# Kernel optimization log

Measured on AMD Instinct MI355X. Metric: run time of the kernel, lower is better.

## Reference

```python
import jax, jax.numpy as jnp
import numpy as np

B, S = 32, 4096
HID, MEM, ATT = 512, 512, 512


def setup_inputs() -> dict:
    key = jax.random.key(0)
    k1, k2, k3, k4, k5, k6, k7 = jax.random.split(key, 7)
    scale_h = 1.0 / np.sqrt(HID)
    scale_m = 1.0 / np.sqrt(MEM)
    scale_a = 1.0 / np.sqrt(ATT)
    return {
        "hidden": jax.random.normal(k1, (B, HID), dtype=jnp.float32),
        "memory": jax.random.normal(k2, (B, S, MEM), dtype=jnp.float32),
        "mem_pad": jnp.zeros((B, S), dtype=jnp.bool_),
        "coverage": jax.random.uniform(k3, (B, S), dtype=jnp.float32),
        # params stored as (in, out) so x @ W == torch Linear(x)
        "W_h": jax.random.uniform(k4, (HID, ATT), minval=-scale_h, maxval=scale_h, dtype=jnp.float32),
        "W_m": jax.random.uniform(k5, (MEM, ATT), minval=-scale_m, maxval=scale_m, dtype=jnp.float32),
        "W_c": jax.random.uniform(k6, (ATT,), minval=-1.0, maxval=1.0, dtype=jnp.float32),
        "v": jax.random.uniform(k7, (ATT,), minval=-scale_a, maxval=scale_a, dtype=jnp.float32),
    }


def reference(hidden, memory, mem_pad, coverage, W_h, W_m, W_c, v):
    h = hidden @ W_h                                   # (B, A)
    m = jnp.einsum('bsd,da->bsa', memory, W_m)         # (B, S, A)
    c_feat = coverage[..., None] * W_c                 # (B, S, A) ; Linear(1->A) == scalar * weight row
    score = jnp.einsum('bsa,a->bs', jnp.tanh(h[:, None, :] + m + c_feat), v)  # (B, S)
    score = jnp.where(mem_pad, -jnp.inf, score)
    attn_weights = jax.nn.softmax(score, axis=-1)      # (B, S)
    context = jnp.einsum('bs,bsd->bd', attn_weights, memory)  # (B, D)
    return context, attn_weights
```

## Files before the change

### kernel.cpp

```cpp
#include <hip/hip_runtime.h>
#include <hip/hip_bf16.h>
#include <math.h>

#define BB 32
#define SS 4096
#define DMEM 512
#define DATT 512

typedef short short8 __attribute__((ext_vector_type(8)));
typedef float floatx4 __attribute__((ext_vector_type(4)));

__device__ inline short f2bf(float x) {
    unsigned u = __float_as_uint(x);
    unsigned r = (u + 0x7fffu + ((u >> 16) & 1u)) >> 16;
    return (short)(r & 0xffffu);
}

__device__ inline float fast_tanh(float x) {
    float e = __expf(2.0f * x);
    float r = __builtin_amdgcn_rcpf(e + 1.0f);
    return __builtin_fmaf(-2.0f, r, 1.0f);
}

__device__ inline void gld_lds16(const void* g, void* l) {
    __builtin_amdgcn_global_load_lds(
        (const __attribute__((address_space(1))) unsigned int*)g,
        (__attribute__((address_space(3))) unsigned int*)l, 16, 0, 0);
}


__global__ void prep_wt_kernel(const float* __restrict__ Wm, short* __restrict__ Wt) {
    const int n0 = blockIdx.x * 32;
    const int k0 = blockIdx.y * 32;
    const int t = threadIdx.x;
    const int r = t >> 5, c = t & 31;
    __shared__ float lds[32 * 33];
#pragma unroll
    for (int j = 0; j < 4; ++j) {
        int kk = r + j * 8;
        lds[kk * 33 + c] = Wm[(size_t)(k0 + kk) * 512 + n0 + c];
    }
    __syncthreads();
#pragma unroll
    for (int j = 0; j < 4; ++j) {
        int nn = r + j * 8;
        Wt[(size_t)(n0 + nn) * 512 + k0 + c] = f2bf(lds[c * 33 + nn]);
    }
}

__global__ void prep_h_kernel(const float* __restrict__ hidden, const float* __restrict__ Wh,
                              float* __restrict__ h) {
    const int b = blockIdx.x;
    const int n = blockIdx.y * 256 + threadIdx.x;
    const int kc = blockIdx.z;
    float acc = 0.f;
#pragma unroll 8
    for (int k = kc * 128; k < kc * 128 + 128; ++k)
        acc += hidden[b * 512 + k] * Wh[(size_t)k * 512 + n];
    atomicAdd(&h[b * 512 + n], acc);
}


__global__ __launch_bounds__(1024, 4)
void fused_kernel(const float* __restrict__ memory,
                  const float* __restrict__ coverage,
                  const unsigned char* __restrict__ pad,
                  const short* __restrict__ Wt,
                  const float* __restrict__ h,
                  const float* __restrict__ Wc,
                  const float* __restrict__ v,
                  float* __restrict__ pOut,
                  float* __restrict__ mWS,
                  float* __restrict__ lWS,
                  float* __restrict__ ctxPart) {
    const int blk = blockIdx.x;
    const int b = blk >> 5;
    const int st = blk & 31;
    const int s0 = st * 128;

    const int tid = threadIdx.x;
    const int lane = tid & 63;
    const int wave = tid >> 6;
    const int wm = wave & 1;
    const int wn = wave >> 1;
    const int col = lane & 15;
    const int q = lane >> 4;

    __shared__ __align__(16) char smem[79368];
    char* tileB0 = smem;
    char* tileB1 = smem + 32768;
    char* tileA  = smem + 65536;
    float* covS   = (float*)(smem + 73728);
    float* sred   = (float*)(smem + 74240);
    float* scoreS = (float*)(smem + 78336);
    float* pS     = (float*)(smem + 78848);
    float* mlS    = (float*)(smem + 79360);
    float4* red4  = (float4*)smem;

    if (tid < 128) covS[tid] = coverage[(size_t)b * SS + s0 + tid];

    const float4* gA4 = (const float4*)(memory + ((size_t)b * SS + s0) * 512);
    const char* gB = (const char*)Wt;

    const int arow = tid >> 3, al8 = tid & 7;
    const int aoff = arow * 64 + (((al8 >> 1) ^ ((arow >> 1) & 3)) << 4) + ((al8 & 1) << 3);
    float4 apf;

    floatx4 acc[4][4];
#pragma unroll
    for (int mi = 0; mi < 4; ++mi)
#pragma unroll
        for (int ni = 0; ni < 4; ++ni)
            acc[mi][ni] = (floatx4){0.f, 0.f, 0.f, 0.f};

    apf = gA4[(size_t)arow * 128 + al8];
#pragma unroll
    for (int it = 0; it < 2; ++it) {
        int ci = it * 1024 + tid;
        int row = ci >> 2;
        int gch = (ci & 3) ^ ((row >> 1) & 3);
        gld_lds16(gB + (size_t)row * 1024 + gch * 16,
                  tileB0 + it * 16384 + wave * 1024);
    }
    {
        union { __hip_bfloat162 h2; unsigned u; } p0, p1;
        p0.h2 = __float22bfloat162_rn(make_float2(apf.x, apf.y));
        p1.h2 = __float22bfloat162_rn(make_float2(apf.z, apf.w));
        uint2 w; w.x = p0.u; w.y = p1.u;
        *(uint2*)(tileA + aoff) = w;
    }
    __syncthreads();

    for (int kt = 0; kt < 16; ++kt) {
        if (kt < 15) {
            apf = gA4[(size_t)arow * 128 + (kt + 1) * 8 + al8];
            char* ldsB = ((kt + 1) & 1) ? tileB1 : tileB0;
#pragma unroll
            for (int it = 0; it < 2; ++it) {
                int ci = it * 1024 + tid;
                int row = ci >> 2;
                int gch = (ci & 3) ^ ((row >> 1) & 3);
                gld_lds16(gB + (size_t)row * 1024 + (kt + 1) * 64 + gch * 16,
                          ldsB + it * 16384 + wave * 1024);
            }
        }

        const char* bbase = (kt & 1) ? tileB1 : tileB0;
        short8 af[4], bf[4];
#pragma unroll
        for (int mi = 0; mi < 4; ++mi) {
            int row = wm * 64 + mi * 16 + col;
            af[mi] = *(const short8*)(tileA + row * 64 + ((q ^ ((row >> 1) & 3)) << 4));
        }
#pragma unroll
        for (int ni = 0; ni < 4; ++ni) {
            int row = wn * 64 + ni * 16 + col;
            bf[ni] = *(const short8*)(bbase + row * 64 + ((q ^ ((row >> 1) & 3)) << 4));
        }
#pragma unroll
        for (int mi = 0; mi < 4; ++mi)
#pragma unroll
            for (int ni = 0; ni < 4; ++ni)
                acc[mi][ni] = __builtin_amdgcn_mfma_f32_16x16x32_bf16(af[mi], bf[ni], acc[mi][ni], 0, 0, 0);

        __syncthreads();

        if (kt < 15) {
            union { __hip_bfloat162 h2; unsigned u; } p0, p1;
            p0.h2 = __float22bfloat162_rn(make_float2(apf.x, apf.y));
            p1.h2 = __float22bfloat162_rn(make_float2(apf.z, apf.w));
            uint2 w; w.x = p0.u; w.y = p1.u;
            *(uint2*)(tileA + aoff) = w;
            __syncthreads();
        }
    }

    float hv[4], wcv[4], vv[4];
#pragma unroll
    for (int ni = 0; ni < 4; ++ni) {
        int n = wn * 64 + ni * 16 + col;
        hv[ni] = h[b * 512 + n];
        wcv[ni] = Wc[n];
        vv[ni] = v[n];
    }
    float rowAcc[4][4];
#pragma unroll
    for (int mi = 0; mi < 4; ++mi)
#pragma unroll
        for (int r = 0; r < 4; ++r)
            rowAcc[mi][r] = 0.f;
#pragma unroll
    for (int mi = 0; mi < 4; ++mi) {
#pragma unroll
        for (int r = 0; r < 4; ++r) {
            float cv = covS[wm * 64 + mi * 16 + q * 4 + r];
#pragma unroll
            for (int ni = 0; ni < 4; ++ni) {
                float val = acc[mi][ni][r] + hv[ni] + cv * wcv[ni];
                rowAcc[mi][r] += fast_tanh(val) * vv[ni];
            }
        }
    }
#pragma unroll
    for (int off = 1; off < 16; off <<= 1)
#pragma unroll
        for (int mi = 0; mi < 4; ++mi)
#pragma unroll
            for (int r = 0; r < 4; ++r)
                rowAcc[mi][r] += __shfl_xor(rowAcc[mi][r], off, 64);

    if (col == 0) {
#pragma unroll
        for (int mi = 0; mi < 4; ++mi)
#pragma unroll
            for (int r = 0; r < 4; ++r)
                sred[wn * 128 + wm * 64 + mi * 16 + q * 4 + r] = rowAcc[mi][r];
    }
    __syncthreads();

    if (tid < 128) {
        float sc = 0.f;
#pragma unroll
        for (int w = 0; w < 8; ++w) sc += sred[w * 128 + tid];
        if (pad[(size_t)b * SS + s0 + tid]) sc = -INFINITY;
        scoreS[tid] = sc;
    }
    __syncthreads();
    if (tid < 64) {
        float mx = fmaxf(scoreS[tid], scoreS[tid + 64]);
#pragma unroll
        for (int off = 32; off >= 1; off >>= 1) mx = fmaxf(mx, __shfl_xor(mx, off, 64));
        if (tid == 0) mlS[0] = mx;
    }
    __syncthreads();
    const float mtile = mlS[0];
    if (tid < 128) pS[tid] = __expf(scoreS[tid] - mtile);
    __syncthreads();
    if (tid < 64) {
        float sm = pS[tid] + pS[tid + 64];
#pragma unroll
        for (int off = 32; off >= 1; off >>= 1) sm += __shfl_xor(sm, off, 64);
        if (tid == 0) mlS[1] = sm;
    }
    __syncthreads();

    if (tid < 128) pOut[(size_t)b * SS + s0 + tid] = pS[tid];
    if (tid == 0) {
        mWS[b * 32 + st] = mtile;
        lWS[b * 32 + st] = mlS[1];
    }

    const int sg = tid >> 7;
    const int dc = tid & 127;
    const float4* m4 = (const float4*)(memory + ((size_t)b * SS + s0) * 512);
    float4 a4 = {0.f, 0.f, 0.f, 0.f};
#pragma unroll 8
    for (int i = 0; i < 16; ++i) {
        int s = sg * 16 + i;
        float w = pS[s];
        float4 f = m4[(size_t)s * 128 + dc];
        a4.x += w * f.x; a4.y += w * f.y; a4.z += w * f.z; a4.w += w * f.w;
    }
    red4[sg * 128 + dc] = a4;
    __syncthreads();
    if (tid < 128) {
        float4 o = {0.f, 0.f, 0.f, 0.f};
#pragma unroll
        for (int g2 = 0; g2 < 8; ++g2) {
            float4 r = red4[g2 * 128 + tid];
            o.x += r.x; o.y += r.y; o.z += r.z; o.w += r.w;
        }
        ((float4*)(ctxPart + ((size_t)(b * 32 + st)) * 512))[tid] = o;
    }
}

__global__ __launch_bounds__(512)
void combine_kernel(const float* __restrict__ mWS,
                    const float* __restrict__ lWS,
                    const float* __restrict__ ctxPart,
                    float* __restrict__ ctx,
                    float* __restrict__ attn) {
    const int b = blockIdx.x;
    const int tid = threadIdx.x;
    __shared__ float scaleS[32];
    __shared__ float gS[2];

    if (tid < 64) {
        float mv = (tid < 32) ? mWS[b * 32 + tid] : -INFINITY;
#pragma unroll
        for (int off = 32; off >= 1; off >>= 1) mv = fmaxf(mv, __shfl_xor(mv, off, 64));
        if (tid == 0) gS[0] = mv;
    }
    __syncthreads();
    const float gmax = gS[0];
    if (tid < 64) {
        float sc = 0.f, lv = 0.f;
        if (tid < 32) {
            sc = __expf(mWS[b * 32 + tid] - gmax);
            scaleS[tid] = sc;
            lv = lWS[b * 32 + tid] * sc;
        }
#pragma unroll
        for (int off = 32; off >= 1; off >>= 1) lv += __shfl_xor(lv, off, 64);
        if (tid == 0) gS[1] = lv;
    }
    __syncthreads();
    const float inv = 1.0f / gS[1];

    float facc = 0.f;
#pragma unroll 8
    for (int st = 0; st < 32; ++st)
        facc += ctxPart[((size_t)(b * 32 + st)) * 512 + tid] * scaleS[st];
    ctx[b * 512 + tid] = facc * inv;

#pragma unroll
    for (int j = 0; j < 8; ++j) {
        size_t idx = (size_t)b * SS + j * 512 + tid;
        attn[idx] = attn[idx] * scaleS[(j * 512 + tid) >> 7] * inv;
    }
}

extern "C" void kernel_launch(void* const* d_in, const int* in_sizes, int n_in,
                              void* d_out, int out_size, void* d_ws, size_t ws_size,
                              hipStream_t stream) {
    (void)in_sizes; (void)n_in; (void)out_size; (void)ws_size;
    const float* hidden   = (const float*)d_in[0];
    const float* memory   = (const float*)d_in[1];
    const unsigned char* mem_pad = (const unsigned char*)d_in[2];
    const float* coverage = (const float*)d_in[3];
    const float* Wh       = (const float*)d_in[4];
    const float* Wm       = (const float*)d_in[5];
    const float* Wc       = (const float*)d_in[6];
    const float* v        = (const float*)d_in[7];

    char* ws = (char*)d_ws;
    short* Wt      = (short*)ws;
    float* h       = (float*)(ws + 512 * 1024);
    float* mWS     = (float*)(ws + 576 * 1024);
    float* lWS     = (float*)(ws + 580 * 1024);
    float* ctxPart = (float*)(ws + 584 * 1024);

    float* ctx  = (float*)d_out;
    float* attn = (float*)d_out + BB * 512;

    hipMemsetAsync(h, 0, BB * 512 * sizeof(float), stream);
    prep_wt_kernel<<<dim3(16, 16), dim3(256), 0, stream>>>(Wm, Wt);
    prep_h_kernel<<<dim3(32, 2, 4), dim3(256), 0, stream>>>(hidden, Wh, h);
    fused_kernel<<<dim3(BB * 32), dim3(1024), 0, stream>>>(
        memory, coverage, mem_pad, Wt, h, Wc, v, attn, mWS, lWS, ctxPart);
    combine_kernel<<<dim3(BB), dim3(512), 0, stream>>>(mWS, lWS, ctxPart, ctx, attn);
}
```

Before: 489.6 us.

## Load Wm tiles directly from global into registers and double-buffer A tile

```diff
diff --git a/kernel.cpp b/kernel.cpp
--- a/kernel.cpp
+++ b/kernel.cpp
@@ -20,12 +20,6 @@
     float e = __expf(2.0f * x);
     float r = __builtin_amdgcn_rcpf(e + 1.0f);
     return __builtin_fmaf(-2.0f, r, 1.0f);
-}
-
-__device__ inline void gld_lds16(const void* g, void* l) {
-    __builtin_amdgcn_global_load_lds(
-        (const __attribute__((address_space(1))) unsigned int*)g,
-        (__attribute__((address_space(3))) unsigned int*)l, 16, 0, 0);
 }
 
 
@@ -86,15 +80,14 @@
     const int col = lane & 15;
     const int q = lane >> 4;
 
-    __shared__ __align__(16) char smem[79368];
-    char* tileB0 = smem;
-    char* tileB1 = smem + 32768;
-    char* tileA  = smem + 65536;
-    float* covS   = (float*)(smem + 73728);
-    float* sred   = (float*)(smem + 74240);
-    float* scoreS = (float*)(smem + 78336);
-    float* pS     = (float*)(smem + 78848);
-    float* mlS    = (float*)(smem + 79360);
+    __shared__ __align__(16) char smem[22024];
+    char* bufA0 = smem;
+    char* bufA1 = smem + 8192;
+    float* covS   = (float*)(smem + 16384);
+    float* sred   = (float*)(smem + 16896);
+    float* scoreS = (float*)(smem + 20992);
+    float* pS     = (float*)(smem + 21504);
+    float* mlS    = (float*)(smem + 22016);
     float4* red4  = (float4*)smem;
 
     if (tid < 128) covS[tid] = coverage[(size_t)b * SS + s0 + tid];
@@ -104,7 +97,9 @@
 
     const int arow = tid >> 3, al8 = tid & 7;
     const int aoff = arow * 64 + (((al8 >> 1) ^ ((arow >> 1) & 3)) << 4) + ((al8 & 1) << 3);
-    float4 apf;
+    const int boff0 = (wn * 64 + col) * 1024 + q * 16;
+
+    float4 apfA;
 
     floatx4 acc[4][4];
 #pragma unroll
@@ -113,67 +108,56 @@
         for (int ni = 0; ni < 4; ++ni)
             acc[mi][ni] = (floatx4){0.f, 0.f, 0.f, 0.f};
 
-    apf = gA4[(size_t)arow * 128 + al8];
-#pragma unroll
-    for (int it = 0; it < 2; ++it) {
-        int ci = it * 1024 + tid;
-        int row = ci >> 2;
-        int gch = (ci & 3) ^ ((row >> 1) & 3);
-        gld_lds16(gB + (size_t)row * 1024 + gch * 16,
-                  tileB0 + it * 16384 + wave * 1024);
-    }
+    apfA = gA4[(size_t)arow * 128 + al8];
     {
         union { __hip_bfloat162 h2; unsigned u; } p0, p1;
-        p0.h2 = __float22bfloat162_rn(make_float2(apf.x, apf.y));
-        p1.h2 = __float22bfloat162_rn(make_float2(apf.z, apf.w));
+        p0.h2 = __float22bfloat162_rn(make_float2(apfA.x, apfA.y));
+        p1.h2 = __float22bfloat162_rn(make_float2(apfA.z, apfA.w));
         uint2 w; w.x = p0.u; w.y = p1.u;
-        *(uint2*)(tileA + aoff) = w;
-    }
-    __syncthreads();
-
+        *(uint2*)(bufA0 + aoff) = w;
+    }
+    apfA = gA4[(size_t)arow * 128 + 8 + al8];
+    asm volatile("s_waitcnt lgkmcnt(0)" ::: "memory");
+    __builtin_amdgcn_sched_barrier(0);
+    __builtin_amdgcn_s_barrier();
+
+#pragma unroll
     for (int kt = 0; kt < 16; ++kt) {
+        short8 bfc[4];
+#pragma unroll
+        for (int ni = 0; ni < 4; ++ni)
+            bfc[ni] = *(const short8*)(gB + (size_t)(boff0 + ni * 16384) + kt * 64);
+
         if (kt < 15) {
-            apf = gA4[(size_t)arow * 128 + (kt + 1) * 8 + al8];
-            char* ldsB = ((kt + 1) & 1) ? tileB1 : tileB0;
-#pragma unroll
-            for (int it = 0; it < 2; ++it) {
-                int ci = it * 1024 + tid;
-                int row = ci >> 2;
-                int gch = (ci & 3) ^ ((row >> 1) & 3);
-                gld_lds16(gB + (size_t)row * 1024 + (kt + 1) * 64 + gch * 16,
-                          ldsB + it * 16384 + wave * 1024);
-            }
-        }
-
-        const char* bbase = (kt & 1) ? tileB1 : tileB0;
-        short8 af[4], bf[4];
+            union { __hip_bfloat162 h2; unsigned u; } p0, p1;
+            p0.h2 = __float22bfloat162_rn(make_float2(apfA.x, apfA.y));
+            p1.h2 = __float22bfloat162_rn(make_float2(apfA.z, apfA.w));
+            uint2 w; w.x = p0.u; w.y = p1.u;
+            char* dst = ((kt + 1) & 1) ? bufA1 : bufA0;
+            *(uint2*)(dst + aoff) = w;
+            if (kt < 14)
+                apfA = gA4[(size_t)arow * 128 + (kt + 2) * 8 + al8];
+        }
+
+        const char* abase = (kt & 1) ? bufA1 : bufA0;
+        short8 af[4];
 #pragma unroll
         for (int mi = 0; mi < 4; ++mi) {
             int row = wm * 64 + mi * 16 + col;
-            af[mi] = *(const short8*)(tileA + row * 64 + ((q ^ ((row >> 1) & 3)) << 4));
-        }
-#pragma unroll
-        for (int ni = 0; ni < 4; ++ni) {
-            int row = wn * 64 + ni * 16 + col;
-            bf[ni] = *(const short8*)(bbase + row * 64 + ((q ^ ((row >> 1) & 3)) << 4));
+            af[mi] = *(const short8*)(abase + row * 64 + ((q ^ ((row >> 1) & 3)) << 4));
         }
 #pragma unroll
         for (int mi = 0; mi < 4; ++mi)
 #pragma unroll
             for (int ni = 0; ni < 4; ++ni)
-                acc[mi][ni] = __builtin_amdgcn_mfma_f32_16x16x32_bf16(af[mi], bf[ni], acc[mi][ni], 0, 0, 0);
-
-        __syncthreads();
-
-        if (kt < 15) {
-            union { __hip_bfloat162 h2; unsigned u; } p0, p1;
-            p0.h2 = __float22bfloat162_rn(make_float2(apf.x, apf.y));
-            p1.h2 = __float22bfloat162_rn(make_float2(apf.z, apf.w));
-            uint2 w; w.x = p0.u; w.y = p1.u;
-            *(uint2*)(tileA + aoff) = w;
-            __syncthreads();
-        }
-    }
+                acc[mi][ni] = __builtin_amdgcn_mfma_f32_16x16x32_bf16(af[mi], bfc[ni], acc[mi][ni], 0, 0, 0);
+
+        asm volatile("s_waitcnt lgkmcnt(0)" ::: "memory");
+        __builtin_amdgcn_sched_barrier(0);
+        __builtin_amdgcn_s_barrier();
+    }
+
+    __syncthreads();
 
     float hv[4], wcv[4], vv[4];
 #pragma unroll
```

Measured after the change: 517.0 us. 5.6% more time.
